# Optimization experiments

Measured on AMD Instinct MI355X. Metric: run time of the kernel, lower is better.

Reference implementation:

```python
import jax, jax.numpy as jnp
import numpy as np

VOCAB = 256
D_MODEL = 1792
NUM_LAYERS = 4
D_STATE = 16
D_CONV = 4
EXPAND = 2
D_INNER = EXPAND * D_MODEL            # 3584
DT_RANK = (D_MODEL + 15) // 16        # 112
EPS = 1e-5


def _ln(x, w, b):
    x32 = x.astype(jnp.float32)
    mu = x32.mean(-1, keepdims=True)
    var = ((x32 - mu) ** 2).mean(-1, keepdims=True)
    return (((x32 - mu) * jax.lax.rsqrt(var + EPS)) * w + b)


def _silu(x):
    return x * jax.nn.sigmoid(x)


def _mamba_mixer(x, in_w, cw, cb, xp_w, dt_w, dt_b, A_log, Dp, out_w):
    # x: [B, L, d_model]
    B, L, _ = x.shape
    xz = jnp.einsum('bld,ed->ble', x, in_w)          # [B, L, 2*d_inner]
    xc, z = jnp.split(xz, 2, axis=-1)
    # depthwise causal conv1d over time
    xc = jax.lax.conv_general_dilated(
        xc.swapaxes(1, 2), cw[:, None, :], (1,), [(D_CONV - 1, 0)],
        feature_group_count=D_INNER,
        dimension_numbers=('NCH', 'OIH', 'NCH')).swapaxes(1, 2) + cb
    xc = _silu(xc)
    dbl = jnp.einsum('bld,ed->ble', xc, xp_w)        # [B, L, dt_rank+2*d_state]
    dt = dbl[..., :DT_RANK]
    Bm = dbl[..., DT_RANK:DT_RANK + D_STATE]
    Cm = dbl[..., DT_RANK + D_STATE:]
    dt = jax.nn.softplus(jnp.einsum('blr,dr->bld', dt, dt_w) + dt_b)  # [B,L,d_inner]
    A = -jnp.exp(A_log)                              # [d_inner, d_state]
    dA = jnp.exp(dt[..., None] * A)                  # [B, L, d_inner, d_state]
    dBx = dt[..., None] * Bm[:, :, None, :] * xc[..., None]

    def step(h, t):
        dA_t, dBx_t, C_t = t
        h = dA_t * h + dBx_t                         # [B, d_inner, d_state]
        y = jnp.einsum('bds,bs->bd', h, C_t)
        return h, y

    h0 = jnp.zeros((B, D_INNER, D_STATE), x.dtype)
    _, ys = jax.lax.scan(step, h0, (dA.swapaxes(0, 1), dBx.swapaxes(0, 1), Cm.swapaxes(0, 1)))
    y = ys.swapaxes(0, 1) + Dp * xc                  # [B, L, d_inner]
    y = y * _silu(z)
    return jnp.einsum('bld,od->blo', y, out_w)       # [B, L, d_model]


def setup_inputs() -> dict:
    key = jax.random.key(0)
    ks = jax.random.split(key, 10)
    B, L = 1, 512
    s = 0.02
    input_ids = jax.random.randint(ks[0], (B, L), 0, VOCAB, dtype=jnp.int32)
    embed = jax.random.normal(ks[1], (VOCAB, D_MODEL), jnp.float32) * s
    in_proj_w = jax.random.normal(ks[2], (NUM_LAYERS, 2 * D_INNER, D_MODEL), jnp.float32) * s
    conv_w = jax.random.normal(ks[3], (NUM_LAYERS, D_INNER, D_CONV), jnp.float32) * 0.1
    conv_b = jnp.zeros((NUM_LAYERS, D_INNER), jnp.float32)
    x_proj_w = jax.random.normal(ks[4], (NUM_LAYERS, DT_RANK + 2 * D_STATE, D_INNER), jnp.float32) * s
    dt_proj_w = jax.random.normal(ks[5], (NUM_LAYERS, D_INNER, DT_RANK), jnp.float32) * (DT_RANK ** -0.5)
    u = jax.random.uniform(ks[6], (NUM_LAYERS, D_INNER), jnp.float32)
    dt = jnp.exp(u * (jnp.log(0.1) - jnp.log(0.001)) + jnp.log(0.001))
    dt_proj_b = dt + jnp.log(-jnp.expm1(-dt))        # inverse softplus
    A_log = jnp.log(jnp.broadcast_to(jnp.arange(1, D_STATE + 1, dtype=jnp.float32), (NUM_LAYERS, D_INNER, D_STATE))) + jnp.zeros((NUM_LAYERS, D_INNER, D_STATE), jnp.float32)
    D_skip = jnp.ones((NUM_LAYERS, D_INNER), jnp.float32)
    out_proj_w = jax.random.normal(ks[7], (NUM_LAYERS, D_MODEL, D_INNER), jnp.float32) * s
    norm_w = jnp.ones((NUM_LAYERS, D_MODEL), jnp.float32)
    norm_b = jnp.zeros((NUM_LAYERS, D_MODEL), jnp.float32)
    final_norm_w = jnp.ones((D_MODEL,), jnp.float32)
    final_norm_b = jnp.zeros((D_MODEL,), jnp.float32)
    return dict(input_ids=input_ids, embed=embed, in_proj_w=in_proj_w, conv_w=conv_w,
                conv_b=conv_b, x_proj_w=x_proj_w, dt_proj_w=dt_proj_w, dt_proj_b=dt_proj_b,
                A_log=A_log, D_skip=D_skip, out_proj_w=out_proj_w, norm_w=norm_w,
                norm_b=norm_b, final_norm_w=final_norm_w, final_norm_b=final_norm_b)


def reference(input_ids, embed, in_proj_w, conv_w, conv_b, x_proj_w, dt_proj_w,
              dt_proj_b, A_log, D_skip, out_proj_w, norm_w, norm_b,
              final_norm_w, final_norm_b):
    hidden = embed[input_ids]                        # [B, L, d_model]
    residual = hidden.astype(jnp.float32)            # residual_in_fp32
    for i in range(NUM_LAYERS):
        if i > 0:
            residual = residual + hidden.astype(jnp.float32)
        h = _ln(residual, norm_w[i], norm_b[i])
        hidden = _mamba_mixer(h, in_proj_w[i], conv_w[i], conv_b[i], x_proj_w[i],
                              dt_proj_w[i], dt_proj_b[i], A_log[i], D_skip[i], out_proj_w[i])
    residual = residual + hidden.astype(jnp.float32)
    return _ln(residual, final_norm_w, final_norm_b)
```

## Files before the change

kernel.cpp:

```cpp
#include <hip/hip_runtime.h>
#include <hip/hip_bf16.h>
#include <math.h>

#define D_MODEL 1792
#define D_INNER 3584
#define D_STATE 16
#define D_CONV  4
#define DT_RANK 112
#define NLAYER  4
#define LSEQ    512
#define XPROJ_N (DT_RANK + 2 * D_STATE)
#define KSPLIT  8
#define KCHUNK  (D_INNER / KSPLIT)
#define SCH     32
#define SCL     (LSEQ / SCH)
#define INSPLIT 2
#define OUTSPLIT 4

typedef __attribute__((ext_vector_type(8))) short bf16x8;
typedef __attribute__((ext_vector_type(8))) ushort u16x8;
typedef __attribute__((ext_vector_type(4))) float f32x4;

__device__ __forceinline__ ushort f2bf(float f) {
    unsigned u = __float_as_uint(f);
    unsigned r = (u + 0x7FFFu + ((u >> 16) & 1u)) >> 16;
    return (ushort)r;
}

__global__ __launch_bounds__(256) void wcvt_kernel(const float* __restrict__ in,
                                                   ushort* __restrict__ out, int n8) {
    int idx = blockIdx.x * 256 + threadIdx.x;
    if (idx >= n8) return;
    const f32x4 a = *((const f32x4*)in + (size_t)idx * 2);
    const f32x4 b = *((const f32x4*)in + (size_t)idx * 2 + 1);
    u16x8 v;
    v[0] = f2bf(a[0]); v[1] = f2bf(a[1]); v[2] = f2bf(a[2]); v[3] = f2bf(a[3]);
    v[4] = f2bf(b[0]); v[5] = f2bf(b[1]); v[6] = f2bf(b[2]); v[7] = f2bf(b[3]);
    *(u16x8*)(out + (size_t)idx * 8) = v;
}

__global__ __launch_bounds__(256) void dtcvt_kernel(const float* __restrict__ w,
                                                    ushort* __restrict__ o) {
    const int n8 = NLAYER * D_INNER * 128 / 8;
    int idx = blockIdx.x * 256 + threadIdx.x;
    if (idx >= n8) return;
    int col8 = idx & 15;
    int row  = idx >> 4;
    u16x8 v = {};
    if (col8 < DT_RANK / 8) {
        const float* p = w + (size_t)row * DT_RANK + col8 * 8;
        const f32x4 a = *(const f32x4*)p;
        const f32x4 b = *(const f32x4*)(p + 4);
        v[0] = f2bf(a[0]); v[1] = f2bf(a[1]); v[2] = f2bf(a[2]); v[3] = f2bf(a[3]);
        v[4] = f2bf(b[0]); v[5] = f2bf(b[1]); v[6] = f2bf(b[2]); v[7] = f2bf(b[3]);
    }
    *(u16x8*)(o + (size_t)idx * 8) = v;
}

__global__ __launch_bounds__(256) void embed_kernel(const int* __restrict__ ids,
                                                    const float* __restrict__ embed,
                                                    float* __restrict__ res) {
    int idx = blockIdx.x * 256 + threadIdx.x;
    if (idx >= LSEQ * D_MODEL) return;
    int l = idx / D_MODEL;
    int d = idx - l * D_MODEL;
    res[idx] = embed[(size_t)ids[l] * D_MODEL + d];
}

__global__ __launch_bounds__(256) void add_ln_kernel(float* __restrict__ res,
                                                     const float* __restrict__ hidp,
                                                     const float* __restrict__ w,
                                                     const float* __restrict__ b,
                                                     float* __restrict__ out32,
                                                     ushort* __restrict__ out16,
                                                     int addFlag) {
    const int l = blockIdx.x;
    const int t = threadIdx.x;
    __shared__ float sbuf[8];
    float loc[7];
    float* row = res + (size_t)l * D_MODEL;

    float sum = 0.f;
#pragma unroll
    for (int i = 0; i < 7; ++i) {
        int d = t + i * 256;
        float v = row[d];
        if (addFlag) {
            float hv = 0.f;
#pragma unroll
            for (int z = 0; z < OUTSPLIT; ++z)
                hv += hidp[(size_t)z * LSEQ * D_MODEL + (size_t)l * D_MODEL + d];
            v += hv; row[d] = v;
        }
        loc[i] = v;
        sum += v;
    }
#pragma unroll
    for (int o = 32; o > 0; o >>= 1) sum += __shfl_down(sum, o, 64);
    if ((t & 63) == 0) sbuf[t >> 6] = sum;
    __syncthreads();
    if (t == 0) sbuf[4] = sbuf[0] + sbuf[1] + sbuf[2] + sbuf[3];
    __syncthreads();
    const float mu = sbuf[4] * (1.f / D_MODEL);

    float vs = 0.f;
#pragma unroll
    for (int i = 0; i < 7; ++i) { float d0 = loc[i] - mu; vs += d0 * d0; }
#pragma unroll
    for (int o = 32; o > 0; o >>= 1) vs += __shfl_down(vs, o, 64);
    __syncthreads();
    if ((t & 63) == 0) sbuf[t >> 6] = vs;
    __syncthreads();
    if (t == 0) sbuf[4] = sbuf[0] + sbuf[1] + sbuf[2] + sbuf[3];
    __syncthreads();
    const float rstd = rsqrtf(sbuf[4] * (1.f / D_MODEL) + 1e-5f);

#pragma unroll
    for (int i = 0; i < 7; ++i) {
        int d = t + i * 256;
        float v = (loc[i] - mu) * rstd * w[d] + b[d];
        if (out16) out16[(size_t)l * D_MODEL + d] = f2bf(v);
        else       out32[(size_t)l * D_MODEL + d] = v;
    }
}

template<int ACT, int NSPLIT>
__global__ __launch_bounds__(256) void gemm_mfma(const ushort* __restrict__ A, int lda,
                                                 const ushort* __restrict__ W,
                                                 float* __restrict__ C,
                                                 int N, int K,
                                                 const float* __restrict__ bias) {
    constexpr int BM = 64;
    constexpr int BK = 32;
    __shared__ ushort As[BM * BK];
    __shared__ ushort Bs[128 * BK];

    const int tid  = threadIdx.x;
    const int lane = tid & 63;
    const int wave = tid >> 6;
    const int m0 = blockIdx.y * BM;
    const int n0 = blockIdx.x * 128;
    const int wm = (wave >> 1) * 32;
    const int wn = (wave & 1) * 64;
    const int frow = lane & 15;
    const int fkg  = lane >> 4;
    const int kchunk = K / NSPLIT;
    const int kbase  = blockIdx.z * kchunk;
    const int M = gridDim.y * BM;

    f32x4 acc[2][4] = {};

    for (int it = 0; it < kchunk / BK; ++it) {
        const int k0 = kbase + it * BK;
        {
            int row = tid >> 2;
            int kc  = (tid & 3) * 8;
            __builtin_amdgcn_global_load_lds(
                (const __attribute__((address_space(1))) void*)(A + (size_t)(m0 + row) * lda + k0 + kc),
                (__attribute__((address_space(3))) void*)(As + tid * 8), 16, 0, 0);
        }
#pragma unroll
        for (int i = 0; i < 2; ++i) {
            int c = tid + i * 256;
            int row = c >> 2;
            int kc  = (c & 3) * 8;
            __builtin_amdgcn_global_load_lds(
                (const __attribute__((address_space(1))) void*)(W + (size_t)(n0 + row) * K + k0 + kc),
                (__attribute__((address_space(3))) void*)(Bs + c * 8), 16, 0, 0);
        }
        __syncthreads();

        bf16x8 af[2];
#pragma unroll
        for (int i = 0; i < 2; ++i)
            af[i] = *(const bf16x8*)(As + (wm + i * 16 + frow) * BK + fkg * 8);

#pragma unroll
        for (int j = 0; j < 4; ++j) {
            bf16x8 bb = *(const bf16x8*)(Bs + (wn + j * 16 + frow) * BK + fkg * 8);
#pragma unroll
            for (int i = 0; i < 2; ++i)
                acc[i][j] = __builtin_amdgcn_mfma_f32_16x16x32_bf16(af[i], bb, acc[i][j], 0, 0, 0);
        }
        __syncthreads();
    }

    float bj[4];
    if (ACT) {
#pragma unroll
        for (int j = 0; j < 4; ++j) bj[j] = bias[n0 + wn + frow + j * 16];
    }

    float* Cz = C + (size_t)blockIdx.z * M * N;
#pragma unroll
    for (int i = 0; i < 2; ++i) {
#pragma unroll
        for (int r = 0; r < 4; ++r) {
            int m = m0 + wm + i * 16 + fkg * 4 + r;
            float* cp = Cz + (size_t)m * N + n0 + wn + frow;
#pragma unroll
            for (int j = 0; j < 4; ++j) {
                float v = acc[i][j][r];
                if (ACT) {
                    v += bj[j];
                    v = (v > 20.f) ? v : __logf(1.f + __expf(v));
                }
                cp[j * 16] = v;
            }
        }
    }
}

__global__ __launch_bounds__(256) void xproj_split(const ushort* __restrict__ xcbf,
                                                   const ushort* __restrict__ W,
                                                   float* __restrict__ xpart) {
    __shared__ ushort As[64 * 32];
    __shared__ ushort Ws[16 * 32];
    const int tid  = threadIdx.x;
    const int lane = tid & 63;
    const int wave = tid >> 6;
    const int n0 = blockIdx.x * 16;
    const int m0 = blockIdx.y * 64;
    const int z  = blockIdx.z;
    const int wm = wave * 16;
    const int frow = lane & 15;
    const int fkg  = lane >> 4;
    const int kbase = z * KCHUNK;

    f32x4 acc = {};

    for (int it = 0; it < KCHUNK / 32; ++it) {
        const int k0 = kbase + it * 32;
        {
            int row = tid >> 2;
            int kc  = (tid & 3) * 8;
            __builtin_amdgcn_global_load_lds(
                (const __attribute__((address_space(1))) void*)(xcbf + (size_t)(m0 + row) * D_INNER + k0 + kc),
                (__attribute__((address_space(3))) void*)(As + tid * 8), 16, 0, 0);
        }
        if (tid < 64) {
            int row = tid >> 2;
            int kc  = (tid & 3) * 8;
            __builtin_amdgcn_global_load_lds(
                (const __attribute__((address_space(1))) void*)(W + (size_t)(n0 + row) * D_INNER + k0 + kc),
                (__attribute__((address_space(3))) void*)(Ws + tid * 8), 16, 0, 0);
        }
        __syncthreads();

        bf16x8 af = *(const bf16x8*)(As + (wm + frow) * 32 + fkg * 8);
        bf16x8 bb = *(const bf16x8*)(Ws + frow * 32 + fkg * 8);
        acc = __builtin_amdgcn_mfma_f32_16x16x32_bf16(af, bb, acc, 0, 0, 0);
        __syncthreads();
    }

#pragma unroll
    for (int r = 0; r < 4; ++r) {
        int m = m0 + wm + fkg * 4 + r;
        int n = n0 + frow;
        xpart[((size_t)z * LSEQ + m) * XPROJ_N + n] = acc[r];
    }
}

__global__ __launch_bounds__(256) void xreduce_kernel(const float* __restrict__ xpart,
                                                      float* __restrict__ dbl,
                                                      ushort* __restrict__ dtb) {
    int idx = blockIdx.x * 256 + threadIdx.x;
    if (idx >= LSEQ * XPROJ_N) return;
    int m = idx / XPROJ_N;
    int n = idx - m * XPROJ_N;
    float s = 0.f;
#pragma unroll
    for (int z = 0; z < KSPLIT; ++z)
        s += xpart[(size_t)z * LSEQ * XPROJ_N + idx];
    dbl[idx] = s;
    if (n < DT_RANK)      dtb[m * 128 + n] = f2bf(s);
    else if (n < 128)     dtb[m * 128 + n] = 0;
}

__global__ __launch_bounds__(256) void conv_silu_kernel(const float* __restrict__ xzp,
                                                        const float* __restrict__ cw,
                                                        const float* __restrict__ cb,
                                                        float* __restrict__ xc,
                                                        ushort* __restrict__ xcbf) {
    const size_t SL = (size_t)LSEQ * 2 * D_INNER;
    int idx = blockIdx.x * 256 + threadIdx.x;
    if (idx >= LSEQ * D_INNER) return;
    int l = idx / D_INNER;
    int c = idx - l * D_INNER;
    const float4 w = *reinterpret_cast<const float4*>(cw + (size_t)c * D_CONV);
    float s = cb[c];
    const float wk[4] = {w.x, w.y, w.z, w.w};
#pragma unroll
    for (int k = 0; k < D_CONV; ++k) {
        int ll = l - (D_CONV - 1) + k;
        if (ll >= 0) {
            float v = xzp[(size_t)ll * (2 * D_INNER) + c]
                    + xzp[SL + (size_t)ll * (2 * D_INNER) + c];
            s = fmaf(wk[k], v, s);
        }
    }
    const float sig = 1.f / (1.f + __expf(-s));
    const float v = s * sig;
    xc[idx] = v;
    xcbf[idx] = f2bf(v);
}

__global__ __launch_bounds__(256) void scan_part1(const float* __restrict__ dt,
                                                  const float* __restrict__ xc,
                                                  const float* __restrict__ dbl,
                                                  const float* __restrict__ A_log,
                                                  float* __restrict__ P,
                                                  float* __restrict__ F) {
    const int d = blockIdx.x * 256 + threadIdx.x;
    const int c = blockIdx.y;
    __shared__ float Bs[SCL][D_STATE];
    {
        int t = threadIdx.x;
        int ll = t >> 4, s = t & 15;
        Bs[ll][s] = dbl[(size_t)(c * SCL + ll) * XPROJ_N + DT_RANK + s];
    }
    float A2[D_STATE], h[D_STATE], p[D_STATE];
#pragma unroll
    for (int s = 0; s < D_STATE; ++s) {
        A2[s] = -__expf(A_log[(size_t)d * D_STATE + s]) * 1.4426950408889634f;
        h[s] = 0.f; p[s] = 1.f;
    }
    __syncthreads();

    for (int li0 = 0; li0 < SCL; li0 += 4) {
        float dtv4[4], xcv4[4];
#pragma unroll
        for (int q = 0; q < 4; ++q) {
            const int l = c * SCL + li0 + q;
            dtv4[q] = dt[(size_t)l * D_INNER + d];
            xcv4[q] = xc[(size_t)l * D_INNER + d];
        }
#pragma unroll
        for (int q = 0; q < 4; ++q) {
            const int li = li0 + q;
            const float dtv = dtv4[q];
            const float coef = dtv * xcv4[q];
#pragma unroll
            for (int s = 0; s < D_STATE; ++s) {
                float e = exp2f(dtv * A2[s]);
                h[s] = fmaf(e, h[s], coef * Bs[li][s]);
                p[s] *= e;
            }
        }
    }
    float* Pp = P + ((size_t)c * D_INNER + d) * D_STATE;
    float* Fp = F + ((size_t)c * D_INNER + d) * D_STATE;
#pragma unroll
    for (int v = 0; v < 4; ++v) {
        *(f32x4*)(Pp + v * 4) = *(f32x4*)(p + v * 4);
        *(f32x4*)(Fp + v * 4) = *(f32x4*)(h + v * 4);
    }
}

__global__ __launch_bounds__(256) void scan_fix(const float* __restrict__ P,
                                                const float* __restrict__ F,
                                                float* __restrict__ Hin) {
    const int idx = blockIdx.x * 256 + threadIdx.x;
    if (idx >= D_INNER * D_STATE) return;
    const size_t stride = (size_t)D_INNER * D_STATE;
    float h = 0.f;
#pragma unroll
    for (int c = 0; c < SCH; ++c) {
        Hin[c * stride + idx] = h;
        h = fmaf(P[c * stride + idx], h, F[c * stride + idx]);
    }
}

__global__ __launch_bounds__(256) void scan_part3(const float* __restrict__ dt,
                                                  const float* __restrict__ xc,
                                                  const float* __restrict__ dbl,
                                                  const float* __restrict__ A_log,
                                                  const float* __restrict__ Dp,
                                                  const float* __restrict__ xzp,
                                                  const float* __restrict__ Hin,
                                                  ushort* __restrict__ ybf) {
    const size_t SL = (size_t)LSEQ * 2 * D_INNER;
    const int d = blockIdx.x * 256 + threadIdx.x;
    const int c = blockIdx.y;
    __shared__ float Bs[SCL][D_STATE];
    __shared__ float Cs[SCL][D_STATE];
    {
        int t = threadIdx.x;
        int ll = t >> 4, s = t & 15;
        Bs[ll][s] = dbl[(size_t)(c * SCL + ll) * XPROJ_N + DT_RANK + s];
        Cs[ll][s] = dbl[(size_t)(c * SCL + ll) * XPROJ_N + DT_RANK + D_STATE + s];
    }
    float A2[D_STATE], h[D_STATE];
#pragma unroll
    for (int s = 0; s < D_STATE; ++s)
        A2[s] = -__expf(A_log[(size_t)d * D_STATE + s]) * 1.4426950408889634f;
    {
        const float* Hp = Hin + ((size_t)c * D_INNER + d) * D_STATE;
#pragma unroll
        for (int v = 0; v < 4; ++v)
            *(f32x4*)(h + v * 4) = *(const f32x4*)(Hp + v * 4);
    }
    const float Dd = Dp[d];
    __syncthreads();

    for (int li0 = 0; li0 < SCL; li0 += 4) {
        float dtv4[4], xcv4[4], zv4[4];
#pragma unroll
        for (int q = 0; q < 4; ++q) {
            const int l = c * SCL + li0 + q;
            dtv4[q] = dt[(size_t)l * D_INNER + d];
            xcv4[q] = xc[(size_t)l * D_INNER + d];
            zv4[q]  = xzp[(size_t)l * (2 * D_INNER) + D_INNER + d]
                    + xzp[SL + (size_t)l * (2 * D_INNER) + D_INNER + d];
        }
#pragma unroll
        for (int q = 0; q < 4; ++q) {
            const int li = li0 + q;
            const float dtv = dtv4[q];
            const float xcv = xcv4[q];
            const float coef = dtv * xcv;
            float a0 = 0.f, a1 = 0.f, a2 = 0.f, a3 = 0.f;
#pragma unroll
            for (int s = 0; s < D_STATE; s += 4) {
                float e0 = exp2f(dtv * A2[s + 0]);
                float e1 = exp2f(dtv * A2[s + 1]);
                float e2 = exp2f(dtv * A2[s + 2]);
                float e3 = exp2f(dtv * A2[s + 3]);
                h[s + 0] = fmaf(e0, h[s + 0], coef * Bs[li][s + 0]);
                h[s + 1] = fmaf(e1, h[s + 1], coef * Bs[li][s + 1]);
                h[s + 2] = fmaf(e2, h[s + 2], coef * Bs[li][s + 2]);
                h[s + 3] = fmaf(e3, h[s + 3], coef * Bs[li][s + 3]);
                a0 = fmaf(h[s + 0], Cs[li][s + 0], a0);
                a1 = fmaf(h[s + 1], Cs[li][s + 1], a1);
                a2 = fmaf(h[s + 2], Cs[li][s + 2], a2);
                a3 = fmaf(h[s + 3], Cs[li][s + 3], a3);
            }
            const float zv = zv4[q];
            const float sig = 1.f / (1.f + __expf(-zv));
            const float y = ((a0 + a1) + (a2 + a3) + Dd * xcv) * (zv * sig);
            ybf[(size_t)(c * SCL + li) * D_INNER + d] = f2bf(y);
        }
    }
}

extern "C" void kernel_launch(void* const* d_in, const int* in_sizes, int n_in,
                              void* d_out, int out_size, void* d_ws, size_t ws_size,
                              hipStream_t stream) {
    const int*   ids       = (const int*)d_in[0];
    const float* embed     = (const float*)d_in[1];
    const float* in_proj_w = (const float*)d_in[2];
    const float* conv_w    = (const float*)d_in[3];
    const float* conv_b    = (const float*)d_in[4];
    const float* x_proj_w  = (const float*)d_in[5];
    const float* dt_proj_w = (const float*)d_in[6];
    const float* dt_proj_b = (const float*)d_in[7];
    const float* A_log     = (const float*)d_in[8];
    const float* D_skip    = (const float*)d_in[9];
    const float* out_proj_w= (const float*)d_in[10];
    const float* norm_w    = (const float*)d_in[11];
    const float* norm_b    = (const float*)d_in[12];
    const float* fin_w     = (const float*)d_in[13];
    const float* fin_b     = (const float*)d_in[14];
    float* out = (float*)d_out;

    float* ws = (float*)d_ws;
    float* res    = ws; ws += LSEQ * D_MODEL;
    float* xzp    = ws; ws += (size_t)INSPLIT * LSEQ * 2 * D_INNER;
    float* xc     = ws; ws += (size_t)LSEQ * D_INNER;
    float* dbl    = ws; ws += LSEQ * XPROJ_N;
    float* dty    = ws; ws += (size_t)LSEQ * D_INNER;
    float* xpart  = ws; ws += (size_t)KSPLIT * LSEQ * XPROJ_N;
    float* Pbuf   = ws; ws += (size_t)SCH * D_INNER * D_STATE;
    float* Fbuf   = ws; ws += (size_t)SCH * D_INNER * D_STATE;
    float* HinB   = ws; ws += (size_t)SCH * D_INNER * D_STATE;
    ushort* hbf   = (ushort*)ws; ws += (LSEQ * D_MODEL) / 2;
    ushort* ybf   = (ushort*)ws; ws += (LSEQ * D_INNER) / 2;
    ushort* xcbf  = (ushort*)ws; ws += (LSEQ * D_INNER) / 2;
    ushort* dtb   = (ushort*)ws; ws += (LSEQ * 128) / 2;
    ushort* inw_bf  = (ushort*)ws; ws += (size_t)NLAYER * 2 * D_INNER * D_MODEL / 2;
    ushort* outw_bf = (ushort*)ws; ws += (size_t)NLAYER * D_MODEL * D_INNER / 2;
    ushort* xw_bf   = (ushort*)ws; ws += (size_t)NLAYER * XPROJ_N * D_INNER / 2;
    ushort* dtw_bf  = (ushort*)ws; ws += (size_t)NLAYER * D_INNER * 128 / 2;
    float* outp = Pbuf;

    {
        int n8_in  = NLAYER * 2 * D_INNER * D_MODEL / 8;
        int n8_out = NLAYER * D_MODEL * D_INNER / 8;
        int n8_x   = NLAYER * XPROJ_N * D_INNER / 8;
        int n8_dt  = NLAYER * D_INNER * 128 / 8;
        wcvt_kernel<<<(n8_in + 255) / 256, 256, 0, stream>>>(in_proj_w, inw_bf, n8_in);
        wcvt_kernel<<<(n8_out + 255) / 256, 256, 0, stream>>>(out_proj_w, outw_bf, n8_out);
        wcvt_kernel<<<(n8_x + 255) / 256, 256, 0, stream>>>(x_proj_w, xw_bf, n8_x);
        dtcvt_kernel<<<(n8_dt + 255) / 256, 256, 0, stream>>>(dt_proj_w, dtw_bf);
    }

    embed_kernel<<<(LSEQ * D_MODEL + 255) / 256, 256, 0, stream>>>(ids, embed, res);

    for (int i = 0; i < NLAYER; ++i) {
        add_ln_kernel<<<LSEQ, 256, 0, stream>>>(
            res, outp, norm_w + (size_t)i * D_MODEL, norm_b + (size_t)i * D_MODEL,
            nullptr, hbf, i > 0 ? 1 : 0);

        gemm_mfma<0, INSPLIT><<<dim3(2 * D_INNER / 128, LSEQ / 64, INSPLIT), 256, 0, stream>>>(
            hbf, D_MODEL, inw_bf + (size_t)i * 2 * D_INNER * D_MODEL, xzp,
            2 * D_INNER, D_MODEL, nullptr);

        conv_silu_kernel<<<(LSEQ * D_INNER + 255) / 256, 256, 0, stream>>>(
            xzp, conv_w + (size_t)i * D_INNER * D_CONV, conv_b + (size_t)i * D_INNER,
            xc, xcbf);

        xproj_split<<<dim3(XPROJ_N / 16, LSEQ / 64, KSPLIT), 256, 0, stream>>>(
            xcbf, xw_bf + (size_t)i * XPROJ_N * D_INNER, xpart);
        xreduce_kernel<<<(LSEQ * XPROJ_N + 255) / 256, 256, 0, stream>>>(xpart, dbl, dtb);

        gemm_mfma<1, 1><<<dim3(D_INNER / 128, LSEQ / 64, 1), 256, 0, stream>>>(
            dtb, 128, dtw_bf + (size_t)i * D_INNER * 128, dty,
            D_INNER, 128, dt_proj_b + (size_t)i * D_INNER);

        scan_part1<<<dim3(D_INNER / 256, SCH), 256, 0, stream>>>(
            dty, xc, dbl, A_log + (size_t)i * D_INNER * D_STATE, Pbuf, Fbuf);
        scan_fix<<<(D_INNER * D_STATE + 255) / 256, 256, 0, stream>>>(Pbuf, Fbuf, HinB);
        scan_part3<<<dim3(D_INNER / 256, SCH), 256, 0, stream>>>(
            dty, xc, dbl, A_log + (size_t)i * D_INNER * D_STATE,
            D_skip + (size_t)i * D_INNER, xzp, HinB, ybf);

        gemm_mfma<0, OUTSPLIT><<<dim3(D_MODEL / 128, LSEQ / 64, OUTSPLIT), 256, 0, stream>>>(
            ybf, D_INNER, outw_bf + (size_t)i * D_MODEL * D_INNER, outp,
            D_MODEL, D_INNER, nullptr);
    }

    add_ln_kernel<<<LSEQ, 256, 0, stream>>>(res, outp, fin_w, fin_b, out, nullptr, 1);
}
```

Baseline: 971.5 us.

## Use 128x128 GEMM tiles, merge weight conversion, fuse embed into LN, vectorize conv

Adds a 128x128-tile MFMA GEMM with direct global-to-LDS loads for the in-projection and out-projection, doubling per-block reuse of A and W tiles. It also merges the four weight-conversion launches into one kernel, folds the embedding gather into the first add+LayerNorm, and vectorizes the conv+SiLU kernel to process four channels per thread. The larger tiles halve the grid size, which may reduce occupancy and wave count on a large-CU GPU.

```diff
diff --git a/kernel.cpp b/kernel.cpp
--- a/kernel.cpp
+++ b/kernel.cpp
@@ -19,6 +19,7 @@
 
 typedef __attribute__((ext_vector_type(8))) short bf16x8;
 typedef __attribute__((ext_vector_type(8))) ushort u16x8;
+typedef __attribute__((ext_vector_type(4))) ushort u16x4;
 typedef __attribute__((ext_vector_type(4))) float f32x4;
 
 __device__ __forceinline__ ushort f2bf(float f) {
@@ -27,44 +28,46 @@
     return (ushort)r;
 }
 
-__global__ __launch_bounds__(256) void wcvt_kernel(const float* __restrict__ in,
-                                                   ushort* __restrict__ out, int n8) {
+__global__ __launch_bounds__(256) void wcvt_all(const float* __restrict__ in_w,
+                                                const float* __restrict__ out_w,
+                                                const float* __restrict__ x_w,
+                                                const float* __restrict__ dt_w,
+                                                ushort* __restrict__ inb,
+                                                ushort* __restrict__ outb,
+                                                ushort* __restrict__ xb,
+                                                ushort* __restrict__ dtwb) {
+    const int n8_in  = NLAYER * 2 * D_INNER * D_MODEL / 8;
+    const int n8_out = NLAYER * D_MODEL * D_INNER / 8;
+    const int n8_x   = NLAYER * XPROJ_N * D_INNER / 8;
+    const int n8_dt  = NLAYER * D_INNER * 128 / 8;
     int idx = blockIdx.x * 256 + threadIdx.x;
-    if (idx >= n8) return;
-    const f32x4 a = *((const f32x4*)in + (size_t)idx * 2);
-    const f32x4 b = *((const f32x4*)in + (size_t)idx * 2 + 1);
+
+    const float* src; ushort* dst; int j;
+    if (idx < n8_in)                          { src = in_w;  dst = inb;  j = idx; }
+    else if (idx < n8_in + n8_out)            { src = out_w; dst = outb; j = idx - n8_in; }
+    else if (idx < n8_in + n8_out + n8_x)     { src = x_w;   dst = xb;   j = idx - n8_in - n8_out; }
+    else if (idx < n8_in + n8_out + n8_x + n8_dt) {
+        j = idx - n8_in - n8_out - n8_x;
+        int col8 = j & 15;
+        int row  = j >> 4;
+        u16x8 v = {};
+        if (col8 < DT_RANK / 8) {
+            const float* p = dt_w + (size_t)row * DT_RANK + col8 * 8;
+            const f32x4 a = *(const f32x4*)p;
+            const f32x4 b = *(const f32x4*)(p + 4);
+            v[0] = f2bf(a[0]); v[1] = f2bf(a[1]); v[2] = f2bf(a[2]); v[3] = f2bf(a[3]);
+            v[4] = f2bf(b[0]); v[5] = f2bf(b[1]); v[6] = f2bf(b[2]); v[7] = f2bf(b[3]);
+        }
+        *(u16x8*)(dtwb + (size_t)j * 8) = v;
+        return;
+    } else return;
+
+    const f32x4 a = *((const f32x4*)src + (size_t)j * 2);
+    const f32x4 b = *((const f32x4*)src + (size_t)j * 2 + 1);
     u16x8 v;
     v[0] = f2bf(a[0]); v[1] = f2bf(a[1]); v[2] = f2bf(a[2]); v[3] = f2bf(a[3]);
     v[4] = f2bf(b[0]); v[5] = f2bf(b[1]); v[6] = f2bf(b[2]); v[7] = f2bf(b[3]);
-    *(u16x8*)(out + (size_t)idx * 8) = v;
-}
-
-__global__ __launch_bounds__(256) void dtcvt_kernel(const float* __restrict__ w,
-                                                    ushort* __restrict__ o) {
-    const int n8 = NLAYER * D_INNER * 128 / 8;
-    int idx = blockIdx.x * 256 + threadIdx.x;
-    if (idx >= n8) return;
-    int col8 = idx & 15;
-    int row  = idx >> 4;
-    u16x8 v = {};
-    if (col8 < DT_RANK / 8) {
-        const float* p = w + (size_t)row * DT_RANK + col8 * 8;
-        const f32x4 a = *(const f32x4*)p;
-        const f32x4 b = *(const f32x4*)(p + 4);
-        v[0] = f2bf(a[0]); v[1] = f2bf(a[1]); v[2] = f2bf(a[2]); v[3] = f2bf(a[3]);
-        v[4] = f2bf(b[0]); v[5] = f2bf(b[1]); v[6] = f2bf(b[2]); v[7] = f2bf(b[3]);
-    }
-    *(u16x8*)(o + (size_t)idx * 8) = v;
-}
-
-__global__ __launch_bounds__(256) void embed_kernel(const int* __restrict__ ids,
-                                                    const float* __restrict__ embed,
-                                                    float* __restrict__ res) {
-    int idx = blockIdx.x * 256 + threadIdx.x;
-    if (idx >= LSEQ * D_MODEL) return;
-    int l = idx / D_MODEL;
-    int d = idx - l * D_MODEL;
-    res[idx] = embed[(size_t)ids[l] * D_MODEL + d];
+    *(u16x8*)(dst + (size_t)j * 8) = v;
 }
 
 __global__ __launch_bounds__(256) void add_ln_kernel(float* __restrict__ res,
@@ -73,24 +76,32 @@
                                                      const float* __restrict__ b,
                                                      float* __restrict__ out32,
                                                      ushort* __restrict__ out16,
-                                                     int addFlag) {
+                                                     int mode,
+                                                     const int* __restrict__ ids,
+                                                     const float* __restrict__ embed) {
     const int l = blockIdx.x;
     const int t = threadIdx.x;
     __shared__ float sbuf[8];
     float loc[7];
     float* row = res + (size_t)l * D_MODEL;
+    const float* erow = (mode == 2) ? (embed + (size_t)ids[l] * D_MODEL) : nullptr;
 
     float sum = 0.f;
 #pragma unroll
     for (int i = 0; i < 7; ++i) {
         int d = t + i * 256;
-        float v = row[d];
-        if (addFlag) {
-            float hv = 0.f;
-#pragma unroll
-            for (int z = 0; z < OUTSPLIT; ++z)
-                hv += hidp[(size_t)z * LSEQ * D_MODEL + (size_t)l * D_MODEL + d];
-            v += hv; row[d] = v;
+        float v;
+        if (mode == 2) {
+            v = erow[d]; row[d] = v;
+        } else {
+            v = row[d];
+            if (mode == 1) {
+                float hv = 0.f;
+#pragma unroll
+                for (int z = 0; z < OUTSPLIT; ++z)
+                    hv += hidp[(size_t)z * LSEQ * D_MODEL + (size_t)l * D_MODEL + d];
+                v += hv; row[d] = v;
+            }
         }
         loc[i] = v;
         sum += v;
@@ -121,6 +132,81 @@
         float v = (loc[i] - mu) * rstd * w[d] + b[d];
         if (out16) out16[(size_t)l * D_MODEL + d] = f2bf(v);
         else       out32[(size_t)l * D_MODEL + d] = v;
+    }
+}
+
+template<int NSPLIT>
+__global__ __launch_bounds__(256) void gemm128_mfma(const ushort* __restrict__ A, int lda,
+                                                    const ushort* __restrict__ W,
+                                                    float* __restrict__ C,
+                                                    int N, int K) {
+    constexpr int BK = 32;
+    __shared__ ushort As[128 * BK];
+    __shared__ ushort Bs[128 * BK];
+
+    const int tid  = threadIdx.x;
+    const int lane = tid & 63;
+    const int wave = tid >> 6;
+    const int m0 = blockIdx.y * 128;
+    const int n0 = blockIdx.x * 128;
+    const int wm = (wave >> 1) * 64;
+    const int wn = (wave & 1) * 64;
+    const int frow = lane & 15;
+    const int fkg  = lane >> 4;
+    const int kchunk = K / NSPLIT;
+    const int kbase  = blockIdx.z * kchunk;
+    const int M = gridDim.y * 128;
+
+    f32x4 acc[4][4] = {};
+
+    for (int it = 0; it < kchunk / BK; ++it) {
+        const int k0 = kbase + it * BK;
+#pragma unroll
+        for (int i = 0; i < 2; ++i) {
+            int c = tid + i * 256;
+            int row = c >> 2;
+            int kc  = (c & 3) * 8;
+            __builtin_amdgcn_global_load_lds(
+                (const __attribute__((address_space(1))) void*)(A + (size_t)(m0 + row) * lda + k0 + kc),
+                (__attribute__((address_space(3))) void*)(As + c * 8), 16, 0, 0);
+        }
+#pragma unroll
+        for (int i = 0; i < 2; ++i) {
+            int c = tid + i * 256;
+            int row = c >> 2;
+            int kc  = (c & 3) * 8;
+            __builtin_amdgcn_global_load_lds(
+                (const __attribute__((address_space(1))) void*)(W + (size_t)(n0 + row) * K + k0 + kc),
+                (__attribute__((address_space(3))) void*)(Bs + c * 8), 16, 0, 0);
+        }
+        __syncthreads();
+
+        bf16x8 af[4];
+#pragma unroll
+        for (int i = 0; i < 4; ++i)
+            af[i] = *(const bf16x8*)(As + (wm + i * 16 + frow) * BK + fkg * 8);
+
+#pragma unroll
+        for (int j = 0; j < 4; ++j) {
+            bf16x8 bb = *(const bf16x8*)(Bs + (wn + j * 16 + frow) * BK + fkg * 8);
+#pragma unroll
+            for (int i = 0; i < 4; ++i)
+                acc[i][j] = __builtin_amdgcn_mfma_f32_16x16x32_bf16(af[i], bb, acc[i][j], 0, 0, 0);
+        }
+        __syncthreads();
+    }
+
+    float* Cz = C + (size_t)blockIdx.z * M * N;
+#pragma unroll
+    for (int i = 0; i < 4; ++i) {
+#pragma unroll
+        for (int r = 0; r < 4; ++r) {
+            int m = m0 + wm + i * 16 + fkg * 4 + r;
+            float* cp = Cz + (size_t)m * N + n0 + wn + frow;
+#pragma unroll
+            for (int j = 0; j < 4; ++j)
+                cp[j * 16] = acc[i][j][r];
+        }
     }
 }
 
@@ -284,25 +370,38 @@
                                                         ushort* __restrict__ xcbf) {
     const size_t SL = (size_t)LSEQ * 2 * D_INNER;
     int idx = blockIdx.x * 256 + threadIdx.x;
-    if (idx >= LSEQ * D_INNER) return;
-    int l = idx / D_INNER;
-    int c = idx - l * D_INNER;
-    const float4 w = *reinterpret_cast<const float4*>(cw + (size_t)c * D_CONV);
-    float s = cb[c];
-    const float wk[4] = {w.x, w.y, w.z, w.w};
+    if (idx >= LSEQ * D_INNER / 4) return;
+    int l  = idx / (D_INNER / 4);
+    int c4 = (idx - l * (D_INNER / 4)) * 4;
+
+    const f32x4 wc0 = *(const f32x4*)(cw + (size_t)(c4 + 0) * D_CONV);
+    const f32x4 wc1 = *(const f32x4*)(cw + (size_t)(c4 + 1) * D_CONV);
+    const f32x4 wc2 = *(const f32x4*)(cw + (size_t)(c4 + 2) * D_CONV);
+    const f32x4 wc3 = *(const f32x4*)(cw + (size_t)(c4 + 3) * D_CONV);
+
+    f32x4 s = *(const f32x4*)(cb + c4);
 #pragma unroll
     for (int k = 0; k < D_CONV; ++k) {
         int ll = l - (D_CONV - 1) + k;
         if (ll >= 0) {
-            float v = xzp[(size_t)ll * (2 * D_INNER) + c]
-                    + xzp[SL + (size_t)ll * (2 * D_INNER) + c];
-            s = fmaf(wk[k], v, s);
-        }
-    }
-    const float sig = 1.f / (1.f + __expf(-s));
-    const float v = s * sig;
-    xc[idx] = v;
-    xcbf[idx] = f2bf(v);
+            const f32x4 v0 = *(const f32x4*)(xzp + (size_t)ll * (2 * D_INNER) + c4);
+            const f32x4 v1 = *(const f32x4*)(xzp + SL + (size_t)ll * (2 * D_INNER) + c4);
+            s[0] = fmaf(wc0[k], v0[0] + v1[0], s[0]);
+            s[1] = fmaf(wc1[k], v0[1] + v1[1], s[1]);
+            s[2] = fmaf(wc2[k], v0[2] + v1[2], s[2]);
+            s[3] = fmaf(wc3[k], v0[3] + v1[3], s[3]);
+        }
+    }
+    f32x4 o;
+    u16x4 ob;
+#pragma unroll
+    for (int q = 0; q < 4; ++q) {
+        const float sig = 1.f / (1.f + __expf(-s[q]));
+        o[q] = s[q] * sig;
+        ob[q] = f2bf(o[q]);
+    }
+    *(f32x4*)(xc + (size_t)idx * 4) = o;
+    *(u16x4*)(xcbf + (size_t)idx * 4) = ob;
 }
 
 __global__ __launch_bounds__(256) void scan_part1(const float* __restrict__ dt,
@@ -484,28 +583,23 @@
     float* outp = Pbuf;
 
     {
-        int n8_in  = NLAYER * 2 * D_INNER * D_MODEL / 8;
-        int n8_out = NLAYER * D_MODEL * D_INNER / 8;
-        int n8_x   = NLAYER * XPROJ_N * D_INNER / 8;
-        int n8_dt  = NLAYER * D_INNER * 128 / 8;
-        wcvt_kernel<<<(n8_in + 255) / 256, 256, 0, stream>>>(in_proj_w, inw_bf, n8_in);
-        wcvt_kernel<<<(n8_out + 255) / 256, 256, 0, stream>>>(out_proj_w, outw_bf, n8_out);
-        wcvt_kernel<<<(n8_x + 255) / 256, 256, 0, stream>>>(x_proj_w, xw_bf, n8_x);
-        dtcvt_kernel<<<(n8_dt + 255) / 256, 256, 0, stream>>>(dt_proj_w, dtw_bf);
-    }
-
-    embed_kernel<<<(LSEQ * D_MODEL + 255) / 256, 256, 0, stream>>>(ids, embed, res);
+        const int n8_total = NLAYER * (2 * D_INNER * D_MODEL + D_MODEL * D_INNER
+                                       + XPROJ_N * D_INNER + D_INNER * 128) / 8;
+        wcvt_all<<<(n8_total + 255) / 256, 256, 0, stream>>>(
+            in_proj_w, out_proj_w, x_proj_w, dt_proj_w,
+            inw_bf, outw_bf, xw_bf, dtw_bf);
+    }
 
     for (int i = 0; i < NLAYER; ++i) {
         add_ln_kernel<<<LSEQ, 256, 0, stream>>>(
             res, outp, norm_w + (size_t)i * D_MODEL, norm_b + (size_t)i * D_MODEL,
-            nullptr, hbf, i > 0 ? 1 : 0);
-
-        gemm_mfma<0, INSPLIT><<<dim3(2 * D_INNER / 128, LSEQ / 64, INSPLIT), 256, 0, stream>>>(
+            nullptr, hbf, i > 0 ? 1 : 2, ids, embed);
+
+        gemm128_mfma<INSPLIT><<<dim3(2 * D_INNER / 128, LSEQ / 128, INSPLIT), 256, 0, stream>>>(
             hbf, D_MODEL, inw_bf + (size_t)i * 2 * D_INNER * D_MODEL, xzp,
-            2 * D_INNER, D_MODEL, nullptr);
-
-        conv_silu_kernel<<<(LSEQ * D_INNER + 255) / 256, 256, 0, stream>>>(
+            2 * D_INNER, D_MODEL);
+
+        conv_silu_kernel<<<(LSEQ * D_INNER / 4 + 255) / 256, 256, 0, stream>>>(
             xzp, conv_w + (size_t)i * D_INNER * D_CONV, conv_b + (size_t)i * D_INNER,
             xc, xcbf);
 
@@ -524,10 +618,11 @@
             dty, xc, dbl, A_log + (size_t)i * D_INNER * D_STATE,
             D_skip + (size_t)i * D_INNER, xzp, HinB, ybf);
 
-        gemm_mfma<0, OUTSPLIT><<<dim3(D_MODEL / 128, LSEQ / 64, OUTSPLIT), 256, 0, stream>>>(
+        gemm128_mfma<OUTSPLIT><<<dim3(D_MODEL / 128, LSEQ / 128, OUTSPLIT), 256, 0, stream>>>(
             ybf, D_INNER, outw_bf + (size_t)i * D_MODEL * D_INNER, outp,
-            D_MODEL, D_INNER, nullptr);
-    }
-
-    add_ln_kernel<<<LSEQ, 256, 0, stream>>>(res, outp, fin_w, fin_b, out, nullptr, 1);
-}
+            D_MODEL, D_INNER);
+    }
+
+    add_ln_kernel<<<LSEQ, 256, 0, stream>>>(res, outp, fin_w, fin_b, out, nullptr, 1,
+                                            nullptr, nullptr);
+}
```

Result: slower. 995.6 us (+2.5%).
